# Performance work log

Hardware: AMD Instinct MI355X
Metric: run time of the kernel (lower is better)

## Reference

```python
import jax, jax.numpy as jnp
import numpy as np


def setup_inputs() -> dict:
    key = jax.random.key(0)
    k1, k2, k3, k4 = jax.random.split(key, 4)
    B, T, E, H = 4, 2048, 1024, 16
    hs = E // H
    x = jax.random.normal(k1, (B, T, E), dtype=jnp.float32)
    # per-head projection weights (nn.Linear bias=False, stored as [H, E, head_size])
    s = 1.0 / np.sqrt(E)
    Wq = jax.random.uniform(k2, (H, E, hs), dtype=jnp.float32, minval=-s, maxval=s)
    Wk = jax.random.uniform(k3, (H, E, hs), dtype=jnp.float32, minval=-s, maxval=s)
    Wv = jax.random.uniform(k4, (H, E, hs), dtype=jnp.float32, minval=-s, maxval=s)
    return {"x": x, "Wq": Wq, "Wk": Wk, "Wv": Wv}


def reference(x, Wq, Wk, Wv):
    # x: [B, T, E]; Wq/Wk/Wv: [H, E, hs]
    B, T, E = x.shape
    H = Wq.shape[0]
    q = jnp.einsum('bte,hed->bhtd', x, Wq)
    k = jnp.einsum('bte,hed->bhtd', x, Wk)
    v = jnp.einsum('bte,hed->bhtd', x, Wv)
    scores = jnp.einsum('bhtd,bhsd->bhts', q, k)
    # causal mask applied before scaling (matches original; -inf unaffected by scale)
    causal = jnp.tril(jnp.ones((T, T), dtype=bool))
    scores = jnp.where(causal, scores, -jnp.inf)
    # NOTE: original scales by sqrt(embed_size), not sqrt(head_size)
    scores = scores / jnp.sqrt(jnp.asarray(E, dtype=scores.dtype))
    w = jax.nn.softmax(scores, axis=-1)
    # dropout: eval mode (identity)
    out = jnp.einsum('bhts,bhsd->bhtd', w, v)  # [B,H,T,hs]
    out = jnp.transpose(out, (0, 2, 1, 3)).reshape(B, T, -1)  # concat heads
    return out
```

## Files before the change

kernel.cpp:

```cpp
#include <hip/hip_runtime.h>
#include <cstdint>
#include <cmath>


typedef __attribute__((ext_vector_type(8))) __bf16 bf16x8;
typedef __attribute__((ext_vector_type(4))) __bf16 bf16x4;
typedef __attribute__((ext_vector_type(4))) float f32x4;
typedef __attribute__((ext_vector_type(16))) float f32x16;

#define B_ 4
#define T_ 2048
#define E_ 1024
#define H_ 16
#define HS_ 64

__device__ __forceinline__ f32x4 mfma16(bf16x8 a, bf16x8 b, f32x4 c) {
  return __builtin_amdgcn_mfma_f32_16x16x32_bf16(a, b, c, 0, 0, 0);
}
__device__ __forceinline__ f32x16 mfma32(bf16x8 a, bf16x8 b, f32x16 c) {
  return __builtin_amdgcn_mfma_f32_32x32x16_bf16(a, b, c, 0, 0, 0);
}

__device__ __forceinline__ void gload_lds16(const void* g, void* l) {
  __builtin_amdgcn_global_load_lds(
      (const __attribute__((address_space(1))) unsigned int*)g,
      (__attribute__((address_space(3))) unsigned int*)l,
      16, 0, 0);
}

__device__ __forceinline__ unsigned cvt_pk_bf16(float lo, float hi) {
  unsigned r;
  asm("v_cvt_pk_bf16_f32 %0, %1, %2" : "=v"(r) : "v"(lo), "v"(hi));
  return r;
}
__device__ __forceinline__ void pl32swap(unsigned& a, unsigned& b) {
  asm("v_permlane32_swap_b32 %0, %1" : "+v"(a), "+v"(b));
}

__global__ __launch_bounds__(256) void cvt_x_kernel(const float* __restrict__ x,
                                                    __bf16* __restrict__ xb) {
  int i = (blockIdx.x * 256 + threadIdx.x) * 4;
  float4 v = *(const float4*)(x + i);
  bf16x4 o;
  o[0] = (__bf16)v.x; o[1] = (__bf16)v.y; o[2] = (__bf16)v.z; o[3] = (__bf16)v.w;
  *(bf16x4*)(xb + i) = o;
}

__global__ __launch_bounds__(256) void cvt_w_kernel(const float* __restrict__ Wq,
                                                    const float* __restrict__ Wk,
                                                    const float* __restrict__ Wv,
                                                    __bf16* __restrict__ wt) {
  __shared__ float tile[64][65];
  const int e0 = blockIdx.x * 64;
  const int h = blockIdx.y;
  const int qkv = blockIdx.z;
  const int t = threadIdx.x;
  const float* W = (qkv == 0) ? Wq : (qkv == 1) ? Wk : Wv;
#pragma unroll
  for (int j = 0; j < 4; ++j) {
    int idx = j * 256 + t;
    int d4 = idx & 15, e = idx >> 4;
    float4 v = *(const float4*)&W[((size_t)(h * 1024 + e0 + e)) * 64 + d4 * 4];
    tile[d4 * 4 + 0][e] = v.x;
    tile[d4 * 4 + 1][e] = v.y;
    tile[d4 * 4 + 2][e] = v.z;
    tile[d4 * 4 + 3][e] = v.w;
  }
  __syncthreads();
#pragma unroll
  for (int j = 0; j < 2; ++j) {
    int idx = j * 256 + t;
    int e8 = idx & 7, d = idx >> 3;
    bf16x8 o;
#pragma unroll
    for (int i = 0; i < 8; ++i) o[i] = (__bf16)tile[d][e8 * 8 + i];
    *(bf16x8*)&wt[((size_t)qkv << 20) + (size_t)(h * 64 + d) * 1024 + e0 + e8 * 8] = o;
  }
}

__global__ __launch_bounds__(256) void qkv_gemm_kernel(
    const __bf16* __restrict__ Xb, const __bf16* __restrict__ Wt,
    __bf16* __restrict__ Qb, __bf16* __restrict__ Kb, __bf16* __restrict__ Vt) {
  __shared__ __bf16 As[4][128 * 32];
  __shared__ __bf16 Bs[4][128 * 32];
  const int qkv = blockIdx.z;
  const int m0 = blockIdx.x * 128;
  const int n0 = blockIdx.y * 128;
  const int t = threadIdx.x;
  const int lane = t & 63;
  const int w = t >> 6, wr = w >> 1, wc = w & 1;
  const int g = lane >> 4, c = lane & 15;

  const __bf16* wsrc = Wt + ((size_t)qkv << 20);
  f32x4 acc[4][4] = {};

  const int srow = t >> 2;
  const int cs8 = (((t & 3) ^ (srow & 3)) << 3);
  const __bf16* gA0 = Xb + (size_t)(m0 + srow) * 1024 + cs8;
  const __bf16* gA1 = Xb + (size_t)(m0 + 64 + srow) * 1024 + cs8;
  const __bf16* gB0 = wsrc + (size_t)(n0 + srow) * 1024 + cs8;
  const __bf16* gB1 = wsrc + (size_t)(n0 + 64 + srow) * 1024 + cs8;

  auto stage = [&](int s) {
    const int b = s & 3;
    const int ko = s * 32;
    gload_lds16(gA0 + ko, &As[b][t * 8]);
    gload_lds16(gA1 + ko, &As[b][2048 + t * 8]);
    gload_lds16(gB0 + ko, &Bs[b][t * 8]);
    gload_lds16(gB1 + ko, &Bs[b][2048 + t * 8]);
  };

  stage(0); stage(1); stage(2);

  const int gx = (g ^ (c & 3)) << 3;

#pragma unroll 1
  for (int kt = 0; kt < 32; ++kt) {
    if (kt <= 29) {
      asm volatile("s_waitcnt vmcnt(8)" ::: "memory");
    } else if (kt == 30) {
      asm volatile("s_waitcnt vmcnt(4)" ::: "memory");
    } else {
      asm volatile("s_waitcnt vmcnt(0)" ::: "memory");
    }
    __builtin_amdgcn_sched_barrier(0);
    __builtin_amdgcn_s_barrier();
    if (kt + 3 < 32) stage(kt + 3);

    const __bf16* Ab = &As[kt & 3][0];
    const __bf16* Bb = &Bs[kt & 3][0];
    bf16x8 af[4], bfr[4];
#pragma unroll
    for (int mi = 0; mi < 4; ++mi)
      af[mi] = *(const bf16x8*)&Ab[(wr * 64 + mi * 16 + c) * 32 + gx];
#pragma unroll
    for (int ni = 0; ni < 4; ++ni)
      bfr[ni] = *(const bf16x8*)&Bb[(wc * 64 + ni * 16 + c) * 32 + gx];
    __builtin_amdgcn_s_setprio(1);
#pragma unroll
    for (int mi = 0; mi < 4; ++mi)
#pragma unroll
      for (int ni = 0; ni < 4; ++ni)
        acc[mi][ni] = mfma16(af[mi], bfr[ni], acc[mi][ni]);
    __builtin_amdgcn_s_setprio(0);
    __builtin_amdgcn_sched_barrier(0);
  }

  const int mbase = m0 + wr * 64 + g * 4;
  const int nbase = n0 + wc * 64 + c;
  if (qkv < 2) {
    __bf16* dst = (qkv == 0) ? Qb : Kb;
#pragma unroll
    for (int mi = 0; mi < 4; ++mi) {
#pragma unroll
      for (int ni = 0; ni < 4; ++ni) {
        int n = nbase + ni * 16;
        int h = n >> 6, d = n & 63;
#pragma unroll
        for (int r = 0; r < 4; ++r) {
          int m = mbase + mi * 16 + r;
          int b = m >> 11, tt = m & 2047;
          dst[(((size_t)b * H_ + h) * T_ + tt) * HS_ + d] = (__bf16)acc[mi][ni][r];
        }
      }
    }
  } else {
#pragma unroll
    for (int mi = 0; mi < 4; ++mi) {
      int m = mbase + mi * 16;
      int b = m >> 11, tt = m & 2047;
#pragma unroll
      for (int ni = 0; ni < 4; ++ni) {
        int n = nbase + ni * 16;
        int h = n >> 6, d = n & 63;
        bf16x4 pk;
        pk[0] = (__bf16)acc[mi][ni][0];
        pk[1] = (__bf16)acc[mi][ni][1];
        pk[2] = (__bf16)acc[mi][ni][2];
        pk[3] = (__bf16)acc[mi][ni][3];
        *(bf16x4*)&Vt[(((size_t)b * H_ + h) * HS_ + d) * T_ + tt] = pk;
      }
    }
  }
}

__global__ __launch_bounds__(512) void attn_kernel(
    const __bf16* __restrict__ Qb, const __bf16* __restrict__ Kb,
    const __bf16* __restrict__ Vt, float* __restrict__ out) {
  __shared__ __bf16 Ks[2][64 * 64];
  __shared__ __bf16 Vs[2][64 * 64];

  const int j = blockIdx.x;
  const int g8 = j >> 6;
  const int qt = (g8 < 4) ? (7 - g8) : (g8 - 4);
  const int bh = j & 63;
  const int b = bh >> 4, hh = bh & 15;
  const int t = threadIdx.x;
  const int lane = t & 63, w = t >> 6;
  const int lr = lane & 31, h = lane >> 5;

  const __bf16* Qg = Qb + (size_t)bh * T_ * HS_;
  const __bf16* Kg = Kb + (size_t)bh * T_ * HS_;
  const __bf16* Vg = Vt + (size_t)bh * HS_ * T_;

  const int srow = t >> 3;
  const int scb = ((t & 7) << 4) ^ ((srow & 7) << 4);
  const int kxor = (lr & 7) << 4;

  const float C2 = 0.04508422f;

  const int qbase = qt * 256;
  const int NT = (qt + 1) * 4;
  const int tqg = qbase + w * 32 + lr;

  const __bf16* Qrow = Qg + (size_t)tqg * 64;
  bf16x8 qf0 = *(const bf16x8*)(Qrow + h * 8);
  bf16x8 qf1 = *(const bf16x8*)(Qrow + 16 + h * 8);
  bf16x8 qf2 = *(const bf16x8*)(Qrow + 32 + h * 8);
  bf16x8 qf3 = *(const bf16x8*)(Qrow + 48 + h * 8);

  f32x16 o0 = {}, o1 = {};
  float m_run = -INFINITY, l_run = 0.f;
  int cur = 0;

  gload_lds16((const char*)Kg + (size_t)srow * 128 + scb, (char*)&Ks[0][0] + t * 16);
  gload_lds16((const char*)Vg + (size_t)srow * 4096 + scb, (char*)&Vs[0][0] + t * 16);
  __syncthreads();

#pragma unroll 1
  for (int kt = 0; kt < NT; ++kt) {
    const int kbase = kt * 64;
    if (kt + 1 < NT) {
      const int nb = cur ^ 1;
      gload_lds16((const char*)Kg + (size_t)(kbase + 64 + srow) * 128 + scb,
                  (char*)&Ks[nb][0] + t * 16);
      gload_lds16((const char*)Vg + (size_t)srow * 4096 + (size_t)(kbase + 64) * 2 + scb,
                  (char*)&Vs[nb][0] + t * 16);
    }
    if (kbase <= qbase + w * 32 + 31) {
      const char* KsB = (const char*)&Ks[cur][0];
      const char* VsB = (const char*)&Vs[cur][0];

      f32x16 s0 = {}, s1 = {};
      __builtin_amdgcn_s_setprio(1);
#pragma unroll
      for (int ds = 0; ds < 4; ++ds) {
        bf16x8 k0 = *(const bf16x8*)(KsB + ((lr * 128 + ds * 32 + h * 16) ^ kxor));
        bf16x8 k1 = *(const bf16x8*)(KsB + (((lr + 32) * 128 + ds * 32 + h * 16) ^ kxor));
        bf16x8 qd = (ds == 0) ? qf0 : (ds == 1) ? qf1 : (ds == 2) ? qf2 : qf3;
        s0 = mfma32(k0, qd, s0);
        s1 = mfma32(k1, qd, s1);
      }
      __builtin_amdgcn_s_setprio(0);

      if (kbase + 63 > qbase + w * 32) {
#pragma unroll
        for (int r = 0; r < 16; ++r) {
          int tk0 = kbase + (r & 3) + 8 * (r >> 2) + 4 * h;
          if (tk0 > tqg) s0[r] = -INFINITY;
          if (tk0 + 32 > tqg) s1[r] = -INFINITY;
        }
      }

      float mx = s0[0];
#pragma unroll
      for (int r = 1; r < 16; ++r) mx = fmaxf(mx, s0[r]);
#pragma unroll
      for (int r = 0; r < 16; ++r) mx = fmaxf(mx, s1[r]);
      mx = fmaxf(mx, __shfl_xor(mx, 32));
      if (!__all(mx - m_run <= 256.f)) {
        float mn = fmaxf(m_run, mx);
        float fac = __builtin_amdgcn_exp2f((m_run - mn) * C2);
        l_run *= fac;
#pragma unroll
        for (int r = 0; r < 16; ++r) { o0[r] *= fac; o1[r] *= fac; }
        m_run = mn;
      }
      float sum = 0.f;
#pragma unroll
      for (int r = 0; r < 16; ++r) {
        s0[r] = __builtin_amdgcn_exp2f((s0[r] - m_run) * C2);
        s1[r] = __builtin_amdgcn_exp2f((s1[r] - m_run) * C2);
        sum += s0[r] + s1[r];
      }
      sum += __shfl_xor(sum, 32);
      l_run += sum;

      __builtin_amdgcn_s_setprio(1);
#pragma unroll
      for (int blk = 0; blk < 4; ++blk) {
        f32x16& sv = (blk < 2) ? s0 : s1;
        const int off = (blk & 1) * 8;
        unsigned u0 = cvt_pk_bf16(sv[off + 0], sv[off + 1]);
        unsigned u1 = cvt_pk_bf16(sv[off + 2], sv[off + 3]);
        unsigned u2 = cvt_pk_bf16(sv[off + 4], sv[off + 5]);
        unsigned u3 = cvt_pk_bf16(sv[off + 6], sv[off + 7]);
        pl32swap(u0, u2);
        pl32swap(u1, u3);
        union { unsigned u[4]; bf16x8 v; } pb;
        pb.u[0] = u0; pb.u[1] = u1; pb.u[2] = u2; pb.u[3] = u3;
        bf16x8 v0 = *(const bf16x8*)(VsB + ((lr * 128 + blk * 32 + h * 16) ^ kxor));
        bf16x8 v1 = *(const bf16x8*)(VsB + (((lr + 32) * 128 + blk * 32 + h * 16) ^ kxor));
        o0 = mfma32(v0, pb.v, o0);
        o1 = mfma32(v1, pb.v, o1);
      }
      __builtin_amdgcn_s_setprio(0);
    }
    __syncthreads();
    cur ^= 1;
  }

  const float inv_l = 1.0f / l_run;
  float* orow = out + ((size_t)b * T_ + tqg) * E_ + hh * 64;
#pragma unroll
  for (int d0i = 0; d0i < 2; ++d0i) {
#pragma unroll
    for (int qd = 0; qd < 4; ++qd) {
      float4 v;
      const f32x16& ac = d0i ? o1 : o0;
      v.x = ac[qd * 4 + 0] * inv_l;
      v.y = ac[qd * 4 + 1] * inv_l;
      v.z = ac[qd * 4 + 2] * inv_l;
      v.w = ac[qd * 4 + 3] * inv_l;
      *(float4*)(orow + d0i * 32 + qd * 8 + 4 * h) = v;
    }
  }
}

extern "C" void kernel_launch(void* const* d_in, const int* in_sizes, int n_in,
                              void* d_out, int out_size, void* d_ws, size_t ws_size,
                              hipStream_t stream) {
  const float* x = (const float*)d_in[0];
  const float* Wq = (const float*)d_in[1];
  const float* Wk = (const float*)d_in[2];
  const float* Wv = (const float*)d_in[3];
  float* out = (float*)d_out;

  char* ws = (char*)d_ws;
  __bf16* Xb = (__bf16*)ws;
  __bf16* Wt = (__bf16*)(ws + (16u << 20));
  __bf16* Qb = (__bf16*)(ws + (22u << 20));
  __bf16* Kb = (__bf16*)(ws + (38u << 20));
  __bf16* Vt = (__bf16*)(ws + (54u << 20));

  cvt_x_kernel<<<8192, 256, 0, stream>>>(x, Xb);
  cvt_w_kernel<<<dim3(16, 16, 3), 256, 0, stream>>>(Wq, Wk, Wv, Wt);
  qkv_gemm_kernel<<<dim3(64, 8, 3), 256, 0, stream>>>(Xb, Wt, Qb, Kb, Vt);
  attn_kernel<<<dim3(512), 512, 0, stream>>>(Qb, Kb, Vt, out);
}
```

Measured before the change: 225.9 us.

## Use 3-slot LDS ring with single barrier per iteration in GEMM and attention

The QKV GEMM drops from a 4-buffer, 3-ahead prefetch to a 3-buffer, 2-ahead ring, cutting LDS use so more blocks may fit per CU. The attention kernel goes from double buffering with a trailing __syncthreads to a 3-slot ring with explicit vmcnt waits and one raw s_barrier per iteration, prefetching two tiles ahead. This aims to remove one barrier per tile and hide global latency better. The trade-offs are less prefetch depth in the GEMM, more LDS in attention, and correctness that now depends on the hand-written waitcnt counts.

```diff
diff --git a/kernel.cpp b/kernel.cpp
--- a/kernel.cpp
+++ b/kernel.cpp
@@ -35,6 +35,9 @@
 }
 __device__ __forceinline__ void pl32swap(unsigned& a, unsigned& b) {
   asm("v_permlane32_swap_b32 %0, %1" : "+v"(a), "+v"(b));
+}
+__device__ __forceinline__ void barrier_asm() {
+  asm volatile("s_barrier" ::: "memory");
 }
 
 __global__ __launch_bounds__(256) void cvt_x_kernel(const float* __restrict__ x,
@@ -81,8 +84,8 @@
 __global__ __launch_bounds__(256) void qkv_gemm_kernel(
     const __bf16* __restrict__ Xb, const __bf16* __restrict__ Wt,
     __bf16* __restrict__ Qb, __bf16* __restrict__ Kb, __bf16* __restrict__ Vt) {
-  __shared__ __bf16 As[4][128 * 32];
-  __shared__ __bf16 Bs[4][128 * 32];
+  __shared__ __bf16 As[3][128 * 32];
+  __shared__ __bf16 Bs[3][128 * 32];
   const int qkv = blockIdx.z;
   const int m0 = blockIdx.x * 128;
   const int n0 = blockIdx.y * 128;
@@ -101,34 +104,36 @@
   const __bf16* gB0 = wsrc + (size_t)(n0 + srow) * 1024 + cs8;
   const __bf16* gB1 = wsrc + (size_t)(n0 + 64 + srow) * 1024 + cs8;
 
-  auto stage = [&](int s) {
-    const int b = s & 3;
+  auto stage = [&](int s, int slot) {
     const int ko = s * 32;
-    gload_lds16(gA0 + ko, &As[b][t * 8]);
-    gload_lds16(gA1 + ko, &As[b][2048 + t * 8]);
-    gload_lds16(gB0 + ko, &Bs[b][t * 8]);
-    gload_lds16(gB1 + ko, &Bs[b][2048 + t * 8]);
+    gload_lds16(gA0 + ko, &As[slot][t * 8]);
+    gload_lds16(gA1 + ko, &As[slot][2048 + t * 8]);
+    gload_lds16(gB0 + ko, &Bs[slot][t * 8]);
+    gload_lds16(gB1 + ko, &Bs[slot][2048 + t * 8]);
   };
 
-  stage(0); stage(1); stage(2);
+  stage(0, 0);
+  stage(1, 1);
 
   const int gx = (g ^ (c & 3)) << 3;
+  int slot = 0;
 
 #pragma unroll 1
   for (int kt = 0; kt < 32; ++kt) {
-    if (kt <= 29) {
-      asm volatile("s_waitcnt vmcnt(8)" ::: "memory");
-    } else if (kt == 30) {
+    if (kt < 31) {
       asm volatile("s_waitcnt vmcnt(4)" ::: "memory");
     } else {
       asm volatile("s_waitcnt vmcnt(0)" ::: "memory");
     }
     __builtin_amdgcn_sched_barrier(0);
-    __builtin_amdgcn_s_barrier();
-    if (kt + 3 < 32) stage(kt + 3);
-
-    const __bf16* Ab = &As[kt & 3][0];
-    const __bf16* Bb = &Bs[kt & 3][0];
+    barrier_asm();
+    if (kt + 2 < 32) {
+      int ns = slot + 2; if (ns >= 3) ns -= 3;
+      stage(kt + 2, ns);
+    }
+
+    const __bf16* Ab = &As[slot][0];
+    const __bf16* Bb = &Bs[slot][0];
     bf16x8 af[4], bfr[4];
 #pragma unroll
     for (int mi = 0; mi < 4; ++mi)
@@ -144,6 +149,7 @@
         acc[mi][ni] = mfma16(af[mi], bfr[ni], acc[mi][ni]);
     __builtin_amdgcn_s_setprio(0);
     __builtin_amdgcn_sched_barrier(0);
+    slot = (slot == 2) ? 0 : slot + 1;
   }
 
   const int mbase = m0 + wr * 64 + g * 4;
@@ -187,8 +193,8 @@
 __global__ __launch_bounds__(512) void attn_kernel(
     const __bf16* __restrict__ Qb, const __bf16* __restrict__ Kb,
     const __bf16* __restrict__ Vt, float* __restrict__ out) {
-  __shared__ __bf16 Ks[2][64 * 64];
-  __shared__ __bf16 Vs[2][64 * 64];
+  __shared__ __bf16 Ks[3][64 * 64];
+  __shared__ __bf16 Vs[3][64 * 64];
 
   const int j = blockIdx.x;
   const int g8 = j >> 6;
@@ -207,6 +213,13 @@
   const int scb = ((t & 7) << 4) ^ ((srow & 7) << 4);
   const int kxor = (lr & 7) << 4;
 
+  auto stageKV = [&](int s, int slot) {
+    gload_lds16((const char*)Kg + (size_t)(s * 64 + srow) * 128 + scb,
+                (char*)&Ks[slot][0] + t * 16);
+    gload_lds16((const char*)Vg + (size_t)srow * 4096 + s * 128 + scb,
+                (char*)&Vs[slot][0] + t * 16);
+  };
+
   const float C2 = 0.04508422f;
 
   const int qbase = qt * 256;
@@ -221,25 +234,29 @@
 
   f32x16 o0 = {}, o1 = {};
   float m_run = -INFINITY, l_run = 0.f;
-  int cur = 0;
-
-  gload_lds16((const char*)Kg + (size_t)srow * 128 + scb, (char*)&Ks[0][0] + t * 16);
-  gload_lds16((const char*)Vg + (size_t)srow * 4096 + scb, (char*)&Vs[0][0] + t * 16);
-  __syncthreads();
+
+  stageKV(0, 0);
+  stageKV(1, 1);
+  int slot = 0;
 
 #pragma unroll 1
   for (int kt = 0; kt < NT; ++kt) {
     const int kbase = kt * 64;
     if (kt + 1 < NT) {
-      const int nb = cur ^ 1;
-      gload_lds16((const char*)Kg + (size_t)(kbase + 64 + srow) * 128 + scb,
-                  (char*)&Ks[nb][0] + t * 16);
-      gload_lds16((const char*)Vg + (size_t)srow * 4096 + (size_t)(kbase + 64) * 2 + scb,
-                  (char*)&Vs[nb][0] + t * 16);
-    }
+      asm volatile("s_waitcnt vmcnt(2)" ::: "memory");
+    } else {
+      asm volatile("s_waitcnt vmcnt(0)" ::: "memory");
+    }
+    __builtin_amdgcn_sched_barrier(0);
+    barrier_asm();
+    if (kt + 2 < NT) {
+      int ns = slot + 2; if (ns >= 3) ns -= 3;
+      stageKV(kt + 2, ns);
+    }
+
     if (kbase <= qbase + w * 32 + 31) {
-      const char* KsB = (const char*)&Ks[cur][0];
-      const char* VsB = (const char*)&Vs[cur][0];
+      const char* KsB = (const char*)&Ks[slot][0];
+      const char* VsB = (const char*)&Vs[slot][0];
 
       f32x16 s0 = {}, s1 = {};
       __builtin_amdgcn_s_setprio(1);
@@ -306,8 +323,7 @@
       }
       __builtin_amdgcn_s_setprio(0);
     }
-    __syncthreads();
-    cur ^= 1;
+    slot = (slot == 2) ? 0 : slot + 1;
   }
 
   const float inv_l = 1.0f / l_run;
```

New measurement: 211.9 us. -6.2%, faster.
